# Kernel tuning notes

Measured on AMD Instinct MI355X. Metric: run time of the kernel, lower is better.

The kernel has to match this reference:

```python
import jax, jax.numpy as jnp
import numpy as np

D_MODEL = 1024
NUM_HEADS = 16
HEAD_DIM = D_MODEL // NUM_HEADS


def setup_inputs() -> dict:
    key = jax.random.key(0)
    ks = jax.random.split(key, 9)
    s = 1.0 / np.sqrt(D_MODEL)
    x = jax.random.normal(ks[0], (2, 2048, D_MODEL), dtype=jnp.float32)
    Wq = jax.random.normal(ks[1], (D_MODEL, D_MODEL), dtype=jnp.float32) * s
    Wk = jax.random.normal(ks[2], (D_MODEL, D_MODEL), dtype=jnp.float32) * s
    Wv = jax.random.normal(ks[3], (D_MODEL, D_MODEL), dtype=jnp.float32) * s
    Wo = jax.random.normal(ks[4], (D_MODEL, D_MODEL), dtype=jnp.float32) * s
    bq = jax.random.normal(ks[5], (D_MODEL,), dtype=jnp.float32) * s
    bk = jax.random.normal(ks[6], (D_MODEL,), dtype=jnp.float32) * s
    bv = jax.random.normal(ks[7], (D_MODEL,), dtype=jnp.float32) * s
    bo = jax.random.normal(ks[8], (D_MODEL,), dtype=jnp.float32) * s
    return {"x": x, "Wq": Wq, "bq": bq, "Wk": Wk, "bk": bk, "Wv": Wv, "bv": bv, "Wo": Wo, "bo": bo}


def reference(x, Wq, bq, Wk, bk, Wv, bv, Wo, bo):
    B, S, D = x.shape
    H, Hd = NUM_HEADS, HEAD_DIM
    # QKV projections
    q = (x @ Wq + bq).reshape(B, S, H, Hd).transpose(0, 2, 1, 3)  # [B,H,S,Hd]
    k = (x @ Wk + bk).reshape(B, S, H, Hd).transpose(0, 2, 1, 3)
    v = (x @ Wv + bv).reshape(B, S, H, Hd).transpose(0, 2, 1, 3)
    scores = jnp.einsum("bhqd,bhkd->bhqk", q, k) / jnp.sqrt(jnp.float32(Hd))
    attn = jax.nn.softmax(scores, axis=-1)
    out = jnp.einsum("bhqk,bhkd->bhqd", attn, v)  # [B,H,S,Hd]
    out = out.transpose(0, 2, 1, 3).reshape(B, S, D)
    return out @ Wo + bo
```

## Files before the change

kernel.cpp:

```cpp
#include <hip/hip_runtime.h>
#include <hip/hip_bf16.h>


typedef unsigned short u16;

#define D_MODEL 1024
#define NHEAD 16
#define HDIM 64
#define BATCH 2
#define SEQ 2048
#define MTOT (BATCH * SEQ)

#define QSCALE 0.18033688011112042f

using frag_ab = __attribute__((ext_vector_type(8))) short;
using frag_s4 = __attribute__((ext_vector_type(4))) short;
using frag_cd = __attribute__((ext_vector_type(4))) float;
using f32x2   = __attribute__((ext_vector_type(2))) float;

__device__ __forceinline__ u16 f2u(float f) {
    union { float f; unsigned int i; } x;
    x.f = f;
    unsigned int r = x.i + 0x7fffu + ((x.i >> 16) & 1u);
    return (u16)(r >> 16);
}
__device__ __forceinline__ unsigned int pkrn(float a, float b) {
    union { __hip_bfloat162 h; unsigned int u; } c;
    c.h = __float22bfloat162_rn(float2{a, b});
    return c.u;
}
__device__ __forceinline__ float fexp2(float x) {
#if __has_builtin(__builtin_amdgcn_exp2f)
    return __builtin_amdgcn_exp2f(x);
#else
    float r;
    asm("v_exp_f32 %0, %1" : "=v"(r) : "v"(x));
    return r;
#endif
}

__global__ void prep(const float* __restrict__ W0, const float* __restrict__ W1,
                     const float* __restrict__ W2, const float* __restrict__ W3,
                     const float* __restrict__ X, u16* __restrict__ Wt,
                     u16* __restrict__ Xb) {
    const int z = blockIdx.z;
    const int tx = threadIdx.x, ty = threadIdx.y;
    const int tid = ty * 32 + tx;
    if (z < 4) {
        __shared__ u16 t[32][33];
        const float* W = (z == 0) ? W0 : (z == 1) ? W1 : (z == 2) ? W2 : W3;
        u16* o = Wt + (size_t)z * D_MODEL * D_MODEL;
        int n0 = blockIdx.x * 32, k0 = blockIdx.y * 32;
        #pragma unroll
        for (int i = ty; i < 32; i += 8) t[i][tx] = f2u(W[(size_t)(k0 + i) * D_MODEL + n0 + tx]);
        __syncthreads();
        const int r = tid >> 3, c = tid & 7;
        ushort4 o4;
        o4.x = t[4 * c + 0][r]; o4.y = t[4 * c + 1][r];
        o4.z = t[4 * c + 2][r]; o4.w = t[4 * c + 3][r];
        *(ushort4*)&o[(size_t)(n0 + r) * D_MODEL + k0 + 4 * c] = o4;
    } else {
        size_t base = ((size_t)(blockIdx.y * 32 + blockIdx.x) * 256 + tid) * 16;
        #pragma unroll
        for (int c = 0; c < 4; ++c) {
            float4 v = *(const float4*)&X[base + c * 4];
            ushort4 o;
            o.x = f2u(v.x); o.y = f2u(v.y); o.z = f2u(v.z); o.w = f2u(v.w);
            *(ushort4*)&Xb[base + c * 4] = o;
        }
    }
}

__launch_bounds__(256, 3)
__global__ void gemm_qkvt(const u16* __restrict__ xb, const u16* __restrict__ Wt,
                          const float* __restrict__ bq, const float* __restrict__ bk,
                          const float* __restrict__ bv, u16* __restrict__ QKw,
                          u16* __restrict__ Vtw) {
    constexpr int BK = 64;
    __shared__ __attribute__((aligned(16))) u16 As[128 * BK];
    __shared__ __attribute__((aligned(16))) u16 Bs[128 * BK];

    const int tid = threadIdx.x;
    const int w = tid >> 6;
    const int lane = tid & 63;
    const int lrow = lane & 15, lquad = lane >> 4;
    const size_t WSZ = (size_t)D_MODEL * D_MODEL;

    const int bid0 = blockIdx.x;
    const int bid = (bid0 & 7) * 96 + (bid0 >> 3);
    const bool vt = bid >= 512;
    const int z = vt ? 2 : (bid >> 8);
    const int t = vt ? (bid - 512) : (bid & 255);
    const int n0 = vt ? (t & 31) * 128 : (t & 7) * 128;
    const int m0 = vt ? (t >> 5) * 128 : (t >> 3) * 128;
    const u16* Ap = vt ? (Wt + 2 * WSZ) : xb;
    const u16* Bp = vt ? xb : (Wt + (size_t)z * WSZ);
    const float* bias = vt ? bv : (z ? bk : bq);

    frag_cd acc[4][4];
    #pragma unroll
    for (int i = 0; i < 4; i++)
        #pragma unroll
        for (int j = 0; j < 4; j++) acc[i][j] = (frag_cd){0.f, 0.f, 0.f, 0.f};

    const int wm = (w >> 1) * 64, wn = (w & 1) * 64;

    for (int k0 = 0; k0 < D_MODEL; k0 += BK) {
        __syncthreads();
        #pragma unroll
        for (int it = 0; it < 4; ++it) {
            int c = it * 256 + tid;
            int r = c >> 3, c8 = c & 7;
            const u16* ga = Ap + (size_t)(m0 + r) * D_MODEL + k0 + c8 * 8;
            char* la = (char*)As + (it * 256 + w * 64) * 16;
            __builtin_amdgcn_global_load_lds((const __attribute__((address_space(1))) void*)ga,
                                             (__attribute__((address_space(3))) void*)la, 16, 0, 0);
            const u16* gb = Bp + (size_t)(n0 + r) * D_MODEL + k0 + c8 * 8;
            char* lb = (char*)Bs + (it * 256 + w * 64) * 16;
            __builtin_amdgcn_global_load_lds((const __attribute__((address_space(1))) void*)gb,
                                             (__attribute__((address_space(3))) void*)lb, 16, 0, 0);
        }
        __syncthreads();

        #pragma unroll
        for (int kc = 0; kc < 2; ++kc) {
            frag_ab av[4], bvv[4];
            #pragma unroll
            for (int i = 0; i < 4; i++)
                av[i] = *(const frag_ab*)&As[(wm + i * 16 + lrow) * BK + kc * 32 + lquad * 8];
            #pragma unroll
            for (int j = 0; j < 4; j++)
                bvv[j] = *(const frag_ab*)&Bs[(wn + j * 16 + lrow) * BK + kc * 32 + lquad * 8];
            #pragma unroll
            for (int i = 0; i < 4; i++)
                #pragma unroll
                for (int j = 0; j < 4; j++)
                    acc[i][j] = __builtin_amdgcn_mfma_f32_16x16x32_bf16(av[i], bvv[j], acc[i][j], 0, 0, 0);
        }
    }

    const float scale = (!vt && z == 0) ? QSCALE : 1.0f;
    #pragma unroll
    for (int j = 0; j < 4; j++) {
        int gn = n0 + wn + j * 16 + lrow;
        #pragma unroll
        for (int i = 0; i < 4; i++) {
            #pragma unroll
            for (int rr = 0; rr < 4; ++rr) {
                int gm = m0 + wm + i * 16 + lquad * 4 + rr;
                if (!vt) {
                    float v = (acc[i][j][rr] + bias[gn]) * scale;
                    u16* oz = QKw + (size_t)z * ((size_t)MTOT * D_MODEL);
                    int b = gm >> 11, s = gm & (SEQ - 1);
                    int h = gn >> 6, d = gn & (HDIM - 1);
                    oz[(((size_t)(b * NHEAD + h)) * SEQ + s) * HDIM + d] = f2u(v);
                } else {
                    float v = acc[i][j][rr] + bias[gm];
                    int h = gm >> 6, d = gm & (HDIM - 1);
                    int b = gn >> 11, s = gn & (SEQ - 1);
                    Vtw[(((size_t)(b * NHEAD + h)) * HDIM + d) * SEQ + s] = f2u(v);
                }
            }
        }
    }
}

__launch_bounds__(256, 2)
__global__ void gemm_out(const u16* __restrict__ A, const u16* __restrict__ Wt,
                         const float* __restrict__ bias, float* __restrict__ out) {
    constexpr int BK = 64;
    __shared__ __attribute__((aligned(16))) u16 As[64 * BK];
    __shared__ __attribute__((aligned(16))) u16 Bs[128 * BK];

    const int tid = threadIdx.x;
    const int w = tid >> 6;
    const int lane = tid & 63;
    const int lrow = lane & 15, lquad = lane >> 4;
    const int L0 = blockIdx.y * 8 + blockIdx.x;
    const int L = (L0 & 7) * 64 + (L0 >> 3);
    const int m0 = (L >> 3) * 64, n0 = (L & 7) * 128;

    frag_cd acc[2][4];
    #pragma unroll
    for (int i = 0; i < 2; i++)
        #pragma unroll
        for (int j = 0; j < 4; j++) acc[i][j] = (frag_cd){0.f, 0.f, 0.f, 0.f};

    const int wm = (w >> 1) * 32, wn = (w & 1) * 64;

    for (int k0 = 0; k0 < D_MODEL; k0 += BK) {
        __syncthreads();
        #pragma unroll
        for (int it = 0; it < 2; ++it) {
            int c = it * 256 + tid;
            int r = c >> 3, c8 = c & 7;
            const u16* ga = A + (size_t)(m0 + r) * D_MODEL + k0 + c8 * 8;
            char* la = (char*)As + (it * 256 + w * 64) * 16;
            __builtin_amdgcn_global_load_lds((const __attribute__((address_space(1))) void*)ga,
                                             (__attribute__((address_space(3))) void*)la, 16, 0, 0);
        }
        #pragma unroll
        for (int it = 0; it < 4; ++it) {
            int c = it * 256 + tid;
            int r = c >> 3, c8 = c & 7;
            const u16* gb = Wt + (size_t)(n0 + r) * D_MODEL + k0 + c8 * 8;
            char* lb = (char*)Bs + (it * 256 + w * 64) * 16;
            __builtin_amdgcn_global_load_lds((const __attribute__((address_space(1))) void*)gb,
                                             (__attribute__((address_space(3))) void*)lb, 16, 0, 0);
        }
        __syncthreads();

        #pragma unroll
        for (int kc = 0; kc < 2; ++kc) {
            frag_ab av[2], bvv[4];
            #pragma unroll
            for (int i = 0; i < 2; i++)
                av[i] = *(const frag_ab*)&As[(wm + i * 16 + lrow) * BK + kc * 32 + lquad * 8];
            #pragma unroll
            for (int j = 0; j < 4; j++)
                bvv[j] = *(const frag_ab*)&Bs[(wn + j * 16 + lrow) * BK + kc * 32 + lquad * 8];
            #pragma unroll
            for (int i = 0; i < 2; i++)
                #pragma unroll
                for (int j = 0; j < 4; j++)
                    acc[i][j] = __builtin_amdgcn_mfma_f32_16x16x32_bf16(av[i], bvv[j], acc[i][j], 0, 0, 0);
        }
    }

    #pragma unroll
    for (int j = 0; j < 4; j++) {
        int gn = n0 + wn + j * 16 + lrow;
        float bvf = bias[gn];
        #pragma unroll
        for (int i = 0; i < 2; i++)
            #pragma unroll
            for (int rr = 0; rr < 4; ++rr) {
                int gm = m0 + wm + i * 16 + lquad * 4 + rr;
                out[(size_t)gm * D_MODEL + gn] = acc[i][j][rr] + bvf;
            }
    }
}

__launch_bounds__(512, 8)
__global__ void attn_kernel(const u16* __restrict__ Q, const u16* __restrict__ K,
                            const u16* __restrict__ Vt, u16* __restrict__ O) {
    __shared__ __attribute__((aligned(16))) u16 SMEM[16384];
    u16* Ks = SMEM;
    u16* Vs = SMEM + 8192;

    const int tid = threadIdx.x;
    const int w = tid >> 6;
    const int lane = tid & 63;
    const int lrow = lane & 15, lquad = lane >> 4;
    const int qg = w & 3;
    const int kh = w >> 2;

    const int L = blockIdx.y * 32 + blockIdx.x;
    const int xcd = L & 7, off = L >> 3;
    const int bh = xcd * 4 + (off >> 5);
    const int q0 = (off & 31) * 64;

    const size_t base = (size_t)bh * SEQ * HDIM;
    const u16* Qg = Q + base;
    const u16* Kg = K + base;
    const u16* Vg = Vt + base;

    frag_ab qf[2];
    #pragma unroll
    for (int kc = 0; kc < 2; ++kc)
        qf[kc] = *(const frag_ab*)&Qg[(size_t)(q0 + qg * 16 + lrow) * HDIM + kc * 32 + lquad * 8];

    frag_cd accOT[4];
    #pragma unroll
    for (int df = 0; df < 4; df++) accOT[df] = (frag_cd){0.f, 0.f, 0.f, 0.f};
    f32x2 lacc2 = (f32x2){0.f, 0.f};

    const int c0 = tid, c1 = 512 + tid;
    const u16* gk0 = Kg + ((c0 >> 3) * HDIM + (((c0 & 7) ^ ((c0 >> 3) & 7)) << 3));
    const u16* gk1 = Kg + ((c1 >> 3) * HDIM + (((c1 & 7) ^ ((c1 >> 3) & 7)) << 3));
    const u16* gv0 = Vg + ((size_t)(c0 >> 4) * SEQ + (((c0 & 15) ^ ((c0 >> 4) & 7)) << 3));
    const u16* gv1 = Vg + ((size_t)(c1 >> 4) * SEQ + (((c1 & 15) ^ ((c1 >> 4) & 7)) << 3));
    char* lk0 = (char*)Ks + (0 * 512 + w * 64) * 16;
    char* lk1 = (char*)Ks + (1 * 512 + w * 64) * 16;
    char* lv0 = (char*)Vs + (0 * 512 + w * 64) * 16;
    char* lv1 = (char*)Vs + (1 * 512 + w * 64) * 16;

    const u16* kb0 = Ks + (kh * 64 + lrow) * 64 + (((0 + lquad) ^ (lrow & 7)) << 3);
    const u16* kb1 = Ks + (kh * 64 + lrow) * 64 + (((4 + lquad) ^ (lrow & 7)) << 3);
    const u16* vb[4];
    #pragma unroll
    for (int cm = 0; cm < 4; ++cm) {
        const int gc = ((kh * 4 + cm) << 1) + (lquad >> 1);
        vb[cm] = Vs + lrow * 128 + ((gc ^ (lrow & 7)) << 3) + (lquad & 1) * 4;
    }

    for (int kt = 0; kt < SEQ / 128; ++kt) {
        __syncthreads();
        __builtin_amdgcn_global_load_lds((const __attribute__((address_space(1))) void*)gk0,
                                         (__attribute__((address_space(3))) void*)lk0, 16, 0, 0);
        __builtin_amdgcn_global_load_lds((const __attribute__((address_space(1))) void*)gk1,
                                         (__attribute__((address_space(3))) void*)lk1, 16, 0, 0);
        __builtin_amdgcn_global_load_lds((const __attribute__((address_space(1))) void*)gv0,
                                         (__attribute__((address_space(3))) void*)lv0, 16, 0, 0);
        __builtin_amdgcn_global_load_lds((const __attribute__((address_space(1))) void*)gv1,
                                         (__attribute__((address_space(3))) void*)lv1, 16, 0, 0);
        gk0 += 128 * HDIM; gk1 += 128 * HDIM;
        gv0 += 128;        gv1 += 128;
        __syncthreads();

        #pragma unroll
        for (int ch = 0; ch < 2; ++ch) {
            frag_cd sc[2];
            #pragma unroll
            for (int m = 0; m < 2; m++) sc[m] = (frag_cd){0.f, 0.f, 0.f, 0.f};
            __builtin_amdgcn_s_setprio(1);
            #pragma unroll
            for (int m = 0; m < 2; m++) {
                frag_ab kf0 = *(const frag_ab*)(kb0 + (ch * 2 + m) * 1024);
                sc[m] = __builtin_amdgcn_mfma_f32_16x16x32_bf16(kf0, qf[0], sc[m], 0, 0, 0);
                frag_ab kf1 = *(const frag_ab*)(kb1 + (ch * 2 + m) * 1024);
                sc[m] = __builtin_amdgcn_mfma_f32_16x16x32_bf16(kf1, qf[1], sc[m], 0, 0, 0);
            }
            __builtin_amdgcn_s_setprio(0);

            frag_s4 pk[2];
            #pragma unroll
            for (int m = 0; m < 2; m++) {
                float e0 = fexp2(sc[m][0]), e1 = fexp2(sc[m][1]);
                float e2 = fexp2(sc[m][2]), e3 = fexp2(sc[m][3]);
                f32x2 a = {e0, e1}, b2 = {e2, e3};
                lacc2 += a + b2;
                union { frag_s4 s; unsigned int u[2]; } pu;
                pu.u[0] = pkrn(e0, e1);
                pu.u[1] = pkrn(e2, e3);
                pk[m] = pu.s;
            }

            __builtin_amdgcn_s_setprio(1);
            #pragma unroll
            for (int m = 0; m < 2; m++) {
                const u16* vp = vb[ch * 2 + m];
                #pragma unroll
                for (int df = 0; df < 4; df++) {
                    frag_s4 vf = *(const frag_s4*)(vp + df * 2048);
                    accOT[df] = __builtin_amdgcn_mfma_f32_16x16x16bf16_1k(vf, pk[m], accOT[df], 0, 0, 0);
                }
            }
            __builtin_amdgcn_s_setprio(0);
        }
    }

    float lacc = lacc2[0] + lacc2[1];
    lacc += __shfl_xor(lacc, 16);
    lacc += __shfl_xor(lacc, 32);

    float* comb = (float*)SMEM;
    float* lsum = (float*)SMEM + 64 * 68;
    __syncthreads();
    if (kh) {
        float* crow = comb + (qg * 16 + lrow) * 68;
        #pragma unroll
        for (int df = 0; df < 4; df++)
            *(float4*)&crow[df * 16 + lquad * 4] =
                (float4){accOT[df][0], accOT[df][1], accOT[df][2], accOT[df][3]};
        if (lquad == 0) lsum[qg * 16 + lrow] = lacc;
    }
    __syncthreads();
    if (!kh) {
        const float* crow = comb + (qg * 16 + lrow) * 68;
        #pragma unroll
        for (int df = 0; df < 4; df++) {
            float4 c = *(const float4*)&crow[df * 16 + lquad * 4];
            accOT[df][0] += c.x; accOT[df][1] += c.y;
            accOT[df][2] += c.z; accOT[df][3] += c.w;
        }
        lacc += lsum[qg * 16 + lrow];

        const int b = bh >> 4, h = bh & (NHEAD - 1);
        const int s = q0 + qg * 16 + lrow;
        const float inv = 1.0f / lacc;
        u16* orow = O + ((size_t)(b * SEQ + s)) * D_MODEL + h * HDIM;
        #pragma unroll
        for (int df = 0; df < 4; df++) {
            union { unsigned int u[2]; ushort4 s4; } o;
            o.u[0] = pkrn(accOT[df][0] * inv, accOT[df][1] * inv);
            o.u[1] = pkrn(accOT[df][2] * inv, accOT[df][3] * inv);
            *(ushort4*)&orow[df * 16 + lquad * 4] = o.s4;
        }
    }
}

extern "C" void kernel_launch(void* const* d_in, const int* in_sizes, int n_in,
                              void* d_out, int out_size, void* d_ws, size_t ws_size,
                              hipStream_t stream) {
    const float* x  = (const float*)d_in[0];
    const float* Wq = (const float*)d_in[1];
    const float* bq = (const float*)d_in[2];
    const float* Wk = (const float*)d_in[3];
    const float* bk = (const float*)d_in[4];
    const float* Wv = (const float*)d_in[5];
    const float* bv = (const float*)d_in[6];
    const float* Wo = (const float*)d_in[7];
    const float* bo = (const float*)d_in[8];

    u16* ws = (u16*)d_ws;
    const size_t WSZ = (size_t)D_MODEL * D_MODEL;
    const size_t TSZ = (size_t)MTOT * D_MODEL;
    u16* xb  = ws;
    u16* Wt  = ws + 4 * WSZ;
    u16* QKw = ws + 8 * WSZ;
    u16* Vtw = QKw + 2 * TSZ;
    u16* Aw  = Vtw + TSZ;

    prep<<<dim3(32, 32, 5), dim3(32, 8), 0, stream>>>(Wq, Wk, Wv, Wo, x, Wt, xb);
    gemm_qkvt<<<dim3(768), 256, 0, stream>>>(xb, Wt, bq, bk, bv, QKw, Vtw);
    attn_kernel<<<dim3(32, 32), 512, 0, stream>>>(QKw, QKw + TSZ, Vtw, Aw);
    gemm_out<<<dim3(8, 64), 256, 0, stream>>>(Aw, Wt + 3 * WSZ, bo, (float*)d_out);
}
```

Measured before the change: 211.0 us.

## Process 128 queries per attention block to reuse K/V tiles across two query groups

Each attention workgroup now handles 128 query rows instead of 64: every wave holds two Q fragments and two output accumulators, so each K and V fragment read from LDS feeds two MFMAs. The grid is halved, which halves the global K/V traffic per head. In exchange, register use per wave grows, the launch-bounds occupancy hint drops from 8 to 4, LDS grows to fit the larger combine buffer, and only 512 blocks remain to fill the GPU.

```diff
diff --git a/kernel.cpp b/kernel.cpp
--- a/kernel.cpp
+++ b/kernel.cpp
@@ -241,10 +241,10 @@
     }
 }
 
-__launch_bounds__(512, 8)
+__launch_bounds__(512, 4)
 __global__ void attn_kernel(const u16* __restrict__ Q, const u16* __restrict__ K,
                             const u16* __restrict__ Vt, u16* __restrict__ O) {
-    __shared__ __attribute__((aligned(16))) u16 SMEM[16384];
+    __shared__ __attribute__((aligned(16))) u16 SMEM[17664];
     u16* Ks = SMEM;
     u16* Vs = SMEM + 8192;
 
@@ -255,25 +255,29 @@
     const int qg = w & 3;
     const int kh = w >> 2;
 
-    const int L = blockIdx.y * 32 + blockIdx.x;
+    const int L = blockIdx.y * 16 + blockIdx.x;
     const int xcd = L & 7, off = L >> 3;
-    const int bh = xcd * 4 + (off >> 5);
-    const int q0 = (off & 31) * 64;
+    const int bh = xcd * 4 + (off >> 4);
+    const int q0 = (off & 15) * 128;
 
     const size_t base = (size_t)bh * SEQ * HDIM;
     const u16* Qg = Q + base;
     const u16* Kg = K + base;
     const u16* Vg = Vt + base;
 
-    frag_ab qf[2];
-    #pragma unroll
-    for (int kc = 0; kc < 2; ++kc)
-        qf[kc] = *(const frag_ab*)&Qg[(size_t)(q0 + qg * 16 + lrow) * HDIM + kc * 32 + lquad * 8];
-
-    frag_cd accOT[4];
-    #pragma unroll
-    for (int df = 0; df < 4; df++) accOT[df] = (frag_cd){0.f, 0.f, 0.f, 0.f};
-    f32x2 lacc2 = (f32x2){0.f, 0.f};
+    frag_ab qf[2][2];
+    #pragma unroll
+    for (int g = 0; g < 2; ++g)
+        #pragma unroll
+        for (int kc = 0; kc < 2; ++kc)
+            qf[g][kc] = *(const frag_ab*)&Qg[(size_t)(q0 + (qg + g * 4) * 16 + lrow) * HDIM + kc * 32 + lquad * 8];
+
+    frag_cd accOT[2][4];
+    #pragma unroll
+    for (int g = 0; g < 2; ++g)
+        #pragma unroll
+        for (int df = 0; df < 4; df++) accOT[g][df] = (frag_cd){0.f, 0.f, 0.f, 0.f};
+    f32x2 la0 = (f32x2){0.f, 0.f}, la1 = (f32x2){0.f, 0.f};
 
     const int c0 = tid, c1 = 512 + tid;
     const u16* gk0 = Kg + ((c0 >> 3) * HDIM + (((c0 & 7) ^ ((c0 >> 3) & 7)) << 3));
@@ -309,83 +313,104 @@
         __syncthreads();
 
         #pragma unroll
-        for (int ch = 0; ch < 2; ++ch) {
-            frag_cd sc[2];
-            #pragma unroll
-            for (int m = 0; m < 2; m++) sc[m] = (frag_cd){0.f, 0.f, 0.f, 0.f};
+        for (int cm = 0; cm < 4; ++cm) {
+            frag_cd sc0 = (frag_cd){0.f, 0.f, 0.f, 0.f};
+            frag_cd sc1 = (frag_cd){0.f, 0.f, 0.f, 0.f};
             __builtin_amdgcn_s_setprio(1);
-            #pragma unroll
-            for (int m = 0; m < 2; m++) {
-                frag_ab kf0 = *(const frag_ab*)(kb0 + (ch * 2 + m) * 1024);
-                sc[m] = __builtin_amdgcn_mfma_f32_16x16x32_bf16(kf0, qf[0], sc[m], 0, 0, 0);
-                frag_ab kf1 = *(const frag_ab*)(kb1 + (ch * 2 + m) * 1024);
-                sc[m] = __builtin_amdgcn_mfma_f32_16x16x32_bf16(kf1, qf[1], sc[m], 0, 0, 0);
+            {
+                frag_ab kf0 = *(const frag_ab*)(kb0 + cm * 1024);
+                frag_ab kf1 = *(const frag_ab*)(kb1 + cm * 1024);
+                sc0 = __builtin_amdgcn_mfma_f32_16x16x32_bf16(kf0, qf[0][0], sc0, 0, 0, 0);
+                sc1 = __builtin_amdgcn_mfma_f32_16x16x32_bf16(kf0, qf[1][0], sc1, 0, 0, 0);
+                sc0 = __builtin_amdgcn_mfma_f32_16x16x32_bf16(kf1, qf[0][1], sc0, 0, 0, 0);
+                sc1 = __builtin_amdgcn_mfma_f32_16x16x32_bf16(kf1, qf[1][1], sc1, 0, 0, 0);
             }
             __builtin_amdgcn_s_setprio(0);
 
-            frag_s4 pk[2];
-            #pragma unroll
-            for (int m = 0; m < 2; m++) {
-                float e0 = fexp2(sc[m][0]), e1 = fexp2(sc[m][1]);
-                float e2 = fexp2(sc[m][2]), e3 = fexp2(sc[m][3]);
+            frag_s4 pk0, pk1;
+            {
+                float e0 = fexp2(sc0[0]), e1 = fexp2(sc0[1]);
+                float e2 = fexp2(sc0[2]), e3 = fexp2(sc0[3]);
                 f32x2 a = {e0, e1}, b2 = {e2, e3};
-                lacc2 += a + b2;
+                la0 += a + b2;
                 union { frag_s4 s; unsigned int u[2]; } pu;
                 pu.u[0] = pkrn(e0, e1);
                 pu.u[1] = pkrn(e2, e3);
-                pk[m] = pu.s;
+                pk0 = pu.s;
+            }
+            {
+                float e0 = fexp2(sc1[0]), e1 = fexp2(sc1[1]);
+                float e2 = fexp2(sc1[2]), e3 = fexp2(sc1[3]);
+                f32x2 a = {e0, e1}, b2 = {e2, e3};
+                la1 += a + b2;
+                union { frag_s4 s; unsigned int u[2]; } pu;
+                pu.u[0] = pkrn(e0, e1);
+                pu.u[1] = pkrn(e2, e3);
+                pk1 = pu.s;
             }
 
             __builtin_amdgcn_s_setprio(1);
-            #pragma unroll
-            for (int m = 0; m < 2; m++) {
-                const u16* vp = vb[ch * 2 + m];
+            {
+                const u16* vp = vb[cm];
                 #pragma unroll
                 for (int df = 0; df < 4; df++) {
                     frag_s4 vf = *(const frag_s4*)(vp + df * 2048);
-                    accOT[df] = __builtin_amdgcn_mfma_f32_16x16x16bf16_1k(vf, pk[m], accOT[df], 0, 0, 0);
+                    accOT[0][df] = __builtin_amdgcn_mfma_f32_16x16x16bf16_1k(vf, pk0, accOT[0][df], 0, 0, 0);
+                    accOT[1][df] = __builtin_amdgcn_mfma_f32_16x16x16bf16_1k(vf, pk1, accOT[1][df], 0, 0, 0);
                 }
             }
             __builtin_amdgcn_s_setprio(0);
         }
     }
 
-    float lacc = lacc2[0] + lacc2[1];
-    lacc += __shfl_xor(lacc, 16);
-    lacc += __shfl_xor(lacc, 32);
+    float s0 = la0[0] + la0[1];
+    s0 += __shfl_xor(s0, 16);
+    s0 += __shfl_xor(s0, 32);
+    float s1 = la1[0] + la1[1];
+    s1 += __shfl_xor(s1, 16);
+    s1 += __shfl_xor(s1, 32);
 
     float* comb = (float*)SMEM;
-    float* lsum = (float*)SMEM + 64 * 68;
+    float* lsum = (float*)SMEM + 128 * 68;
     __syncthreads();
     if (kh) {
-        float* crow = comb + (qg * 16 + lrow) * 68;
-        #pragma unroll
-        for (int df = 0; df < 4; df++)
-            *(float4*)&crow[df * 16 + lquad * 4] =
-                (float4){accOT[df][0], accOT[df][1], accOT[df][2], accOT[df][3]};
-        if (lquad == 0) lsum[qg * 16 + lrow] = lacc;
+        #pragma unroll
+        for (int g = 0; g < 2; ++g) {
+            float* crow = comb + ((qg + g * 4) * 16 + lrow) * 68;
+            #pragma unroll
+            for (int df = 0; df < 4; df++)
+                *(float4*)&crow[df * 16 + lquad * 4] =
+                    (float4){accOT[g][df][0], accOT[g][df][1], accOT[g][df][2], accOT[g][df][3]};
+        }
+        if (lquad == 0) {
+            lsum[qg * 16 + lrow] = s0;
+            lsum[(qg + 4) * 16 + lrow] = s1;
+        }
     }
     __syncthreads();
     if (!kh) {
-        const float* crow = comb + (qg * 16 + lrow) * 68;
-        #pragma unroll
-        for (int df = 0; df < 4; df++) {
-            float4 c = *(const float4*)&crow[df * 16 + lquad * 4];
-            accOT[df][0] += c.x; accOT[df][1] += c.y;
-            accOT[df][2] += c.z; accOT[df][3] += c.w;
-        }
-        lacc += lsum[qg * 16 + lrow];
-
         const int b = bh >> 4, h = bh & (NHEAD - 1);
-        const int s = q0 + qg * 16 + lrow;
-        const float inv = 1.0f / lacc;
-        u16* orow = O + ((size_t)(b * SEQ + s)) * D_MODEL + h * HDIM;
-        #pragma unroll
-        for (int df = 0; df < 4; df++) {
-            union { unsigned int u[2]; ushort4 s4; } o;
-            o.u[0] = pkrn(accOT[df][0] * inv, accOT[df][1] * inv);
-            o.u[1] = pkrn(accOT[df][2] * inv, accOT[df][3] * inv);
-            *(ushort4*)&orow[df * 16 + lquad * 4] = o.s4;
+        #pragma unroll
+        for (int g = 0; g < 2; ++g) {
+            const float* crow = comb + ((qg + g * 4) * 16 + lrow) * 68;
+            #pragma unroll
+            for (int df = 0; df < 4; df++) {
+                float4 c = *(const float4*)&crow[df * 16 + lquad * 4];
+                accOT[g][df][0] += c.x; accOT[g][df][1] += c.y;
+                accOT[g][df][2] += c.z; accOT[g][df][3] += c.w;
+            }
+            float lacc = (g ? s1 : s0) + lsum[(qg + g * 4) * 16 + lrow];
+
+            const int s = q0 + (qg + g * 4) * 16 + lrow;
+            const float inv = 1.0f / lacc;
+            u16* orow = O + ((size_t)(b * SEQ + s)) * D_MODEL + h * HDIM;
+            #pragma unroll
+            for (int df = 0; df < 4; df++) {
+                union { unsigned int u[2]; ushort4 s4; } o;
+                o.u[0] = pkrn(accOT[g][df][0] * inv, accOT[g][df][1] * inv);
+                o.u[1] = pkrn(accOT[g][df][2] * inv, accOT[g][df][3] * inv);
+                *(ushort4*)&orow[df * 16 + lquad * 4] = o.s4;
+            }
         }
     }
 }
@@ -414,6 +439,6 @@
 
     prep<<<dim3(32, 32, 5), dim3(32, 8), 0, stream>>>(Wq, Wk, Wv, Wo, x, Wt, xb);
     gemm_qkvt<<<dim3(768), 256, 0, stream>>>(xb, Wt, bq, bk, bv, QKw, Vtw);
-    attn_kernel<<<dim3(32, 32), 512, 0, stream>>>(QKw, QKw + TSZ, Vtw, Aw);
+    attn_kernel<<<dim3(16, 32), 512, 0, stream>>>(QKw, QKw + TSZ, Vtw, Aw);
     gemm_out<<<dim3(8, 64), 256, 0, stream>>>(Aw, Wt + 3 * WSZ, bo, (float*)d_out);
 }
```

New measurement: 208.5 us. About the same (-1.2%).
